# Kernel tuning notes

Measured on AMD Instinct MI355X. Metric: run time of the kernel, lower is better.

The kernel has to match this reference:

```python
import jax, jax.numpy as jnp
import numpy as np

# Dimensions pinned by the module: RelPosEmb1DAISummer(tokens=50, dim_head=124)
H = 8          # num_heads
D = 31         # channels // num_heads
T = 4          # time axis of the (p, t) spatial grid; D*T == 124 == dim_head
P = 50         # tokens
C = H * D      # 248 channels
SCALE = D ** -0.5  # note: module scales by d**-0.5 (=31), not (d*t)**-0.5 -- faithful


def rel_to_abs(x):
    """AI-Summer 1D relative->absolute reindexing. x: [b, h, l, 2l-1] -> [b, h, l, l]."""
    b, h, l, _ = x.shape
    x = jnp.pad(x, ((0, 0), (0, 0), (0, 0), (0, 1)))          # [b,h,l,2l]
    x = x.reshape(b, h, l * 2 * l)
    x = jnp.pad(x, ((0, 0), (0, 0), (0, l - 1)))
    x = x.reshape(b, h, l + 1, 2 * l - 1)
    return x[:, :, :l, l - 1:]


def setup_inputs() -> dict:
    key = jax.random.key(0)
    k1, k2, k3, k4 = jax.random.split(key, 4)
    B = 512
    x = jax.random.normal(k1, (B, C, P, T), jnp.float32)
    # 1x1 conv == per-position linear over channels: weight [3C, C], bias [3C]
    w_qkv = jax.random.normal(k2, (3 * C, C), jnp.float32) * (C ** -0.5)
    b_qkv = jax.random.normal(k3, (3 * C,), jnp.float32) * 0.01
    # shared-heads relative position embedding: [2*tokens-1, dim_head]
    rel_emb = jax.random.normal(k4, (2 * P - 1, D * T), jnp.float32) * ((D * T) ** -0.5)
    return {"x": x, "w_qkv": w_qkv, "b_qkv": b_qkv, "rel_emb": rel_emb}


def reference(x, w_qkv, b_qkv, rel_emb):
    B = x.shape[0]
    # 1x1 Conv2d: [B, C, P, T] -> [B, 3C, P, T]
    qkv = jnp.einsum('bcpt,oc->bopt', x, w_qkv) + b_qkv[None, :, None, None]
    # 'b (qkv h d) p t -> qkv b h d p t'
    qkv = qkv.reshape(B, 3, H, D, P, T)
    q, k, v = qkv[:, 0], qkv[:, 1], qkv[:, 2]                 # each [B,H,D,P,T]
    q = q.transpose(0, 1, 3, 2, 4).reshape(B, H, P, D * T)    # 'b h d p t -> b h p (d t)'
    k = k.transpose(0, 1, 2, 4, 3).reshape(B, H, D * T, P)    # 'b h d p t -> b h (d t) p'
    v = v.transpose(0, 1, 3, 2, 4).reshape(B, H, P, D * T)
    dots = jnp.einsum('bhpi,bhiq->bhpq', q, k)                # [B,H,P,P]
    bias = rel_to_abs(jnp.einsum('bhpd,rd->bhpr', q, rel_emb))
    attn = jax.nn.softmax((dots + bias) * SCALE, axis=-1)     # dropout = identity (eval)
    out = jnp.einsum('bhpq,bhqi->bhpi', attn, v)              # [B,H,P,D*T]
    # 'b h p (d t) -> b (h d) p t'
    out = out.reshape(B, H, P, D, T).transpose(0, 1, 3, 2, 4).reshape(B, H * D, P, T)
    return out
```

## Files before the change

kernel.cpp:

```cpp
#include <hip/hip_runtime.h>
#include <hip/hip_bf16.h>
#include <stdint.h>

typedef __bf16 bf16_t;
typedef bf16_t bf16x8 __attribute__((ext_vector_type(8)));
typedef bf16_t bf16x4 __attribute__((ext_vector_type(4)));
typedef float f32x4 __attribute__((ext_vector_type(4)));

constexpr float SCALE = 0.17960530202677491f;

__device__ __forceinline__ f32x4 mfma16(bf16x8 a, bf16x8 b, f32x4 c) {
    return __builtin_amdgcn_mfma_f32_16x16x32_bf16(a, b, c, 0, 0, 0);
}
__device__ __forceinline__ void fence() {
    asm volatile("s_waitcnt lgkmcnt(0)" ::: "memory");
}
__device__ __forceinline__ void gload_lds16(const void* g, void* l) {
    __builtin_amdgcn_global_load_lds((const __attribute__((address_space(1))) void*)g,
                                     (__attribute__((address_space(3))) void*)l, 16, 0, 0);
}

__global__ void prep_kernel(const float* __restrict__ w, const float* __restrict__ rel,
                            bf16_t* __restrict__ WT, bf16_t* __restrict__ relf)
{
    int i = blockIdx.x * 256 + threadIdx.x;
    if (i < 196608) {
        int o = i >> 8, c = i & 255;
        WT[i] = (o < 744 && c < 248) ? (bf16_t)w[(long)o * 248 + c] : (bf16_t)0.f;
        return;
    }
    i -= 196608;
    if (i < 14336) {
        int e = i & 7, lane = (i >> 3) & 63;
        int f = i >> 9;
        int ks = f & 3, rt = f >> 2;
        int r = rt * 16 + (lane & 15);
        int dt = ks * 32 + (lane >> 4) * 8 + e;
        float v = 0.f;
        if (r < 99 && dt < 124) v = rel[r * 124 + dt];
        relf[i] = (bf16_t)v;
    }
}

__global__ void __launch_bounds__(512)
xb_kernel(const float* __restrict__ x, bf16_t* __restrict__ XT)
{
    __shared__ __align__(16) char XS[31744];
    const int tid = threadIdx.x;
    const int blk = blockIdx.x;
    const int cl = tid & 63;
    const int cg = tid >> 6;
    {
        int f = blk * 64 + cl;
        int b = f / 200;
        int nn = f - b * 200;
        const float* xp = x + (long)b * 49600 + nn;
#pragma unroll
        for (int ii = 0; ii < 4; ++ii) {
            int cb = cg + 8 * ii;
            if (cb < 31) {
                bf16x8 pk;
#pragma unroll
                for (int e = 0; e < 8; ++e)
                    pk[e] = (bf16_t)xp[(long)(cb * 8 + e) * 200];
                *(bf16x8*)(XS + cl * 496 + cb * 16) = pk;
            }
        }
    }
    __syncthreads();
    if (tid < 496) {
        char* dst = (char*)XT + (long)blk * 31744 + tid * 64;
#pragma unroll
        for (int j = 0; j < 4; ++j)
            *(f32x4*)(dst + j * 16) = *(const f32x4*)(XS + tid * 64 + j * 16);
    }
}

__global__ void __launch_bounds__(256)
qkv_kernel(const bf16_t* __restrict__ XT, const bf16_t* __restrict__ WT,
           const float* __restrict__ bqkv, bf16_t* __restrict__ qkv)
{
    __shared__ __align__(16) char SM[32768];
    const int raw = blockIdx.x;
    const int swz = (raw & 7) * 600 + (raw >> 3);
    const int mt = swz % 6, nt = swz / 6;
    const int n0 = nt * 128, o0 = mt * 128;
    const int tid  = threadIdx.x;
    const int lane = tid & 63;
    const int wv   = tid >> 6;
    const int r15  = lane & 15, g4 = lane >> 4;
    const int kc   = lane & 3, rsub = lane >> 2;
    const int wr = wv >> 1, wc = wv & 1;

    f32x4 acc[4][4];
#pragma unroll
    for (int a = 0; a < 4; ++a)
#pragma unroll
        for (int b = 0; b < 4; ++b) acc[a][b] = f32x4{0.f, 0.f, 0.f, 0.f};

    const char* XTb = (const char*)XT;
    const char* WTb = (const char*)WT;

#define STAGE(BUF, KS)                                                          \
    {                                                                           \
        _Pragma("unroll")                                                       \
        for (int i_ = 0; i_ < 2; ++i_) {                                        \
            int r0 = (wv * 2 + i_) * 16;                                        \
            int row = r0 + rsub;                                                \
            gload_lds16(XTb + (long)(n0 + row) * 496 + ((KS) * 4 + kc) * 16,    \
                        SM + (BUF) * 8192 + r0 * 64);                           \
            gload_lds16(WTb + (long)(o0 + row) * 512 + ((KS) * 4 + kc) * 16,    \
                        SM + 16384 + (BUF) * 8192 + r0 * 64);                   \
        }                                                                       \
    }

    STAGE(0, 0);
    __syncthreads();

    int buf = 0;
    for (int ks = 0; ks < 8; ++ks) {
        if (ks < 7) STAGE(buf ^ 1, ks + 1);
        bf16x8 Af[4], Bf[4];
#pragma unroll
        for (int fn = 0; fn < 4; ++fn) {
            int row = wr * 64 + fn * 16 + r15;
            Af[fn] = *(const bf16x8*)(SM + buf * 8192 + row * 64 + g4 * 16);
        }
#pragma unroll
        for (int fo = 0; fo < 4; ++fo) {
            int row = wc * 64 + fo * 16 + r15;
            Bf[fo] = *(const bf16x8*)(SM + 16384 + buf * 8192 + row * 64 + g4 * 16);
        }
#pragma unroll
        for (int fn = 0; fn < 4; ++fn)
#pragma unroll
            for (int fo = 0; fo < 4; ++fo)
                acc[fn][fo] = mfma16(Af[fn], Bf[fo], acc[fn][fo]);
        __syncthreads();
        buf ^= 1;
    }
#undef STAGE

#pragma unroll
    for (int fo = 0; fo < 4; ++fo) {
        int o = o0 + wc * 64 + fo * 16 + r15;
        bool vo = (o < 744);
        int s = (o >= 496) ? 2 : ((o >= 248) ? 1 : 0);
        int rem = o - s * 248;
        int h = rem / 31;
        int d = rem - h * 31;
        float bias = vo ? bqkv[o] : 0.f;
        float sc = (s == 0) ? SCALE : 1.f;
        bf16_t* baseo = qkv + (long)s * 26214400 + d * 4;
#pragma unroll
        for (int fn = 0; fn < 4; ++fn) {
            int n = n0 + wr * 64 + fn * 16 + g4 * 4;
            int b = n / 200;
            int p = (n - b * 200) >> 2;
            if (vo) {
                f32x4 a = acc[fn][fo];
                bf16x4 pk = {(bf16_t)((a[0] + bias) * sc), (bf16_t)((a[1] + bias) * sc),
                             (bf16_t)((a[2] + bias) * sc), (bf16_t)((a[3] + bias) * sc)};
                *(bf16x4*)(baseo + ((long)(b * 8 + h) * 50 + p) * 128) = pk;
            }
        }
    }
}

__global__ void __launch_bounds__(256)
attn_kernel(const bf16_t* __restrict__ qkv, const bf16_t* __restrict__ relf,
            float* __restrict__ out)
{
    __shared__ float LS[50][52];
    __shared__ __align__(16) char AS[8192];
    __shared__ __align__(16) char VT[16384];
    const int bid = blockIdx.x;
    const int bb = bid >> 3, hh = bid & 7;
    const int tid  = threadIdx.x;
    const int lane = tid & 63;
    const int w    = tid >> 6;
    const int r15  = lane & 15, g4 = lane >> 4;

    const bf16_t* qB = qkv + (long)bid * 6400;
    const bf16_t* kB = qkv + 26214400L + (long)bid * 6400;
    const bf16_t* vB = qkv + 52428800L + (long)bid * 6400;

    {
        int p_ = tid >> 2, cc = tid & 3;
#pragma unroll
        for (int u = 0; u < 4; ++u) {
            int c = cc + u * 4;
            bf16x8 vv = *(const bf16x8*)(vB + p_ * 128 + c * 8);
#pragma unroll
            for (int e = 0; e < 8; ++e) {
                int i = c * 8 + e;
                *(bf16_t*)(VT + i * 128 + ((((p_ >> 3) ^ (i & 7))) << 4) + (p_ & 7) * 2) = vv[e];
            }
        }
    }

    bf16x8 Afr[4];
#pragma unroll
    for (int ks = 0; ks < 4; ++ks)
        Afr[ks] = *(const bf16x8*)(qB + (w * 16 + r15) * 128 + ks * 32 + g4 * 8);

#pragma unroll
    for (int ct = 0; ct < 4; ++ct) {
        int c = ct * 16 + r15;
        f32x4 sA = f32x4{0.f, 0.f, 0.f, 0.f};
#pragma unroll
        for (int ks = 0; ks < 4; ++ks) {
            bf16x8 Bf = *(const bf16x8*)(kB + c * 128 + ks * 32 + g4 * 8);
            sA = mfma16(Afr[ks], Bf, sA);
        }
        if (c < 50) {
#pragma unroll
            for (int j = 0; j < 4; ++j) {
                int qrow = w * 16 + g4 * 4 + j;
                if (qrow < 50) LS[qrow][c] = sA[j];
            }
        }
    }
    fence();

    {
        const bf16_t* rf = relf + lane * 8;
        bf16x8 R0[4];
#pragma unroll
        for (int ks = 0; ks < 4; ++ks) R0[ks] = *(const bf16x8*)(rf + (ks << 9));
        for (int rt = 0; rt < 7; ++rt) {
            bf16x8 R1[4];
            if (rt < 6) {
#pragma unroll
                for (int ks = 0; ks < 4; ++ks)
                    R1[ks] = *(const bf16x8*)(rf + (((rt + 1) * 4 + ks) << 9));
            }
            f32x4 sA = f32x4{0.f, 0.f, 0.f, 0.f};
#pragma unroll
            for (int ks = 0; ks < 4; ++ks) sA = mfma16(Afr[ks], R0[ks], sA);
            int r = rt * 16 + r15;
#pragma unroll
            for (int j = 0; j < 4; ++j) {
                int qrow = w * 16 + g4 * 4 + j;
                int jj = r + qrow - 49;
                if (qrow < 50 && jj >= 0 && jj < 50) LS[qrow][jj] += sA[j];
            }
#pragma unroll
            for (int ks = 0; ks < 4; ++ks) R0[ks] = R1[ks];
        }
    }
    fence();

    {
        int row = w * 16 + (lane >> 2);
        int quad = lane & 3;
        int hrow = row & 7;
        if (row < 50) {
            float mx = -1e30f;
            for (int jj = quad; jj < 50; jj += 4) mx = fmaxf(mx, LS[row][jj]);
            mx = fmaxf(mx, __shfl_xor(mx, 1));
            mx = fmaxf(mx, __shfl_xor(mx, 2));
            float sum = 0.f;
            for (int jj = quad; jj < 50; jj += 4) {
                float e = __expf(LS[row][jj] - mx);
                LS[row][jj] = e;
                sum += e;
            }
            sum += __shfl_xor(sum, 1);
            sum += __shfl_xor(sum, 2);
            float rs = 1.f / sum;
            for (int jj = quad; jj < 64; jj += 4) {
                float v = (jj < 50) ? LS[row][jj] * rs : 0.f;
                *(bf16_t*)(AS + row * 128 + (((jj >> 3) ^ hrow) << 4) + (jj & 7) * 2) = (bf16_t)v;
            }
        } else {
            for (int jj = quad; jj < 64; jj += 4)
                *(bf16_t*)(AS + row * 128 + (((jj >> 3) ^ hrow) << 4) + (jj & 7) * 2) = (bf16_t)0.f;
        }
    }
    __syncthreads();

#pragma unroll
    for (int ii = 0; ii < 2; ++ii) {
        int itile = w * 2 + ii;
        int irow = itile * 16 + r15;
        bf16x8 Av[2];
#pragma unroll
        for (int ks = 0; ks < 2; ++ks)
            Av[ks] = *(const bf16x8*)(VT + irow * 128 + ((((ks * 4) + g4) ^ (irow & 7)) << 4));
        int dd = itile * 4 + g4;
#pragma unroll
        for (int pt = 0; pt < 4; ++pt) {
            int prow = pt * 16 + r15;
            int hp2 = prow & 7;
            f32x4 po = f32x4{0.f, 0.f, 0.f, 0.f};
#pragma unroll
            for (int ks = 0; ks < 2; ++ks) {
                bf16x8 Bs = *(const bf16x8*)(AS + prow * 128 + ((((ks * 4) + g4) ^ hp2) << 4));
                po = mfma16(Av[ks], Bs, po);
            }
            if (dd < 31 && prow < 50)
                *(f32x4*)(out + ((long)bb * 248 + hh * 31 + dd) * 200 + prow * 4) = po;
        }
    }
}

extern "C" void kernel_launch(void* const* d_in, const int* in_sizes, int n_in,
                              void* d_out, int out_size, void* d_ws, size_t ws_size,
                              hipStream_t stream)
{
    const float* x   = (const float*)d_in[0];
    const float* wq  = (const float*)d_in[1];
    const float* bq  = (const float*)d_in[2];
    const float* rel = (const float*)d_in[3];
    float* out = (float*)d_out;

    char* ws = (char*)d_ws;
    bf16_t* WT   = (bf16_t*)ws;
    bf16_t* relf = (bf16_t*)(ws + 393216);
    bf16_t* qkv  = (bf16_t*)(ws + 421888);

    bf16_t* XT = (bf16_t*)d_out;

    const int B = in_sizes[0] / 49600;

    prep_kernel<<<dim3(824), dim3(256), 0, stream>>>(wq, rel, WT, relf);
    xb_kernel<<<dim3(B * 200 / 64), dim3(512), 0, stream>>>(x, XT);
    qkv_kernel<<<dim3(4800), dim3(256), 0, stream>>>(XT, WT, bq, qkv);
    attn_kernel<<<dim3(B * 8), dim3(256), 0, stream>>>(qkv, relf, out);
}
```

Measured before the change: 194.8 us.

## Store V pre-transposed from QKV epilogue and defer softmax normalization

The QKV GEMM epilogue now writes V directly in a transposed [bh][dt][p] layout, padded to 64 columns, and the prep kernel zero-fills the padding. This removes the per-block LDS transpose of V in the attention kernel. The softmax no longer writes back normalized values: unnormalized exps go straight into the bf16 A buffer, and the 1/sum scale is applied to the output. The trade-off is scattered 2-byte global stores in the QKV epilogue and an extra zero-fill pass over the vT buffer.

```diff
diff --git a/kernel.cpp b/kernel.cpp
--- a/kernel.cpp
+++ b/kernel.cpp
@@ -21,7 +21,8 @@
 }
 
 __global__ void prep_kernel(const float* __restrict__ w, const float* __restrict__ rel,
-                            bf16_t* __restrict__ WT, bf16_t* __restrict__ relf)
+                            bf16_t* __restrict__ WT, bf16_t* __restrict__ relf,
+                            bf16_t* __restrict__ vT)
 {
     int i = blockIdx.x * 256 + threadIdx.x;
     if (i < 196608) {
@@ -39,6 +40,19 @@
         float v = 0.f;
         if (r < 99 && dt < 124) v = rel[r * 124 + dt];
         relf[i] = (bf16_t)v;
+        return;
+    }
+    i -= 14336;
+    if (i < 524288) {
+        int bh = i >> 7, r = i & 127;
+        char* rb = (char*)(vT + ((long)bh * 128 + r) * 64);
+        f32x4 z = f32x4{0.f, 0.f, 0.f, 0.f};
+        *(f32x4*)(rb + 96)  = z;
+        *(f32x4*)(rb + 112) = z;
+        if (r >= 124) {
+#pragma unroll
+            for (int j = 0; j < 6; ++j) *(f32x4*)(rb + j * 16) = z;
+        }
     }
 }
 
@@ -78,7 +92,8 @@
 
 __global__ void __launch_bounds__(256)
 qkv_kernel(const bf16_t* __restrict__ XT, const bf16_t* __restrict__ WT,
-           const float* __restrict__ bqkv, bf16_t* __restrict__ qkv)
+           const float* __restrict__ bqkv, bf16_t* __restrict__ qk,
+           bf16_t* __restrict__ vT)
 {
     __shared__ __align__(16) char SM[32768];
     const int raw = blockIdx.x;
@@ -151,29 +166,38 @@
         int d = rem - h * 31;
         float bias = vo ? bqkv[o] : 0.f;
         float sc = (s == 0) ? SCALE : 1.f;
-        bf16_t* baseo = qkv + (long)s * 26214400 + d * 4;
 #pragma unroll
         for (int fn = 0; fn < 4; ++fn) {
             int n = n0 + wr * 64 + fn * 16 + g4 * 4;
             int b = n / 200;
             int p = (n - b * 200) >> 2;
+            long bh = (long)(b * 8 + h);
             if (vo) {
                 f32x4 a = acc[fn][fo];
-                bf16x4 pk = {(bf16_t)((a[0] + bias) * sc), (bf16_t)((a[1] + bias) * sc),
-                             (bf16_t)((a[2] + bias) * sc), (bf16_t)((a[3] + bias) * sc)};
-                *(bf16x4*)(baseo + ((long)(b * 8 + h) * 50 + p) * 128) = pk;
+                float a0 = (a[0] + bias) * sc, a1 = (a[1] + bias) * sc;
+                float a2 = (a[2] + bias) * sc, a3 = (a[3] + bias) * sc;
+                if (s < 2) {
+                    bf16x4 pk = {(bf16_t)a0, (bf16_t)a1, (bf16_t)a2, (bf16_t)a3};
+                    *(bf16x4*)(qk + (long)s * 26214400 + (bh * 50 + p) * 128 + d * 4) = pk;
+                } else {
+                    bf16_t* vb2 = vT + (bh * 128 + d * 4) * 64 + p;
+                    vb2[0]   = (bf16_t)a0;
+                    vb2[64]  = (bf16_t)a1;
+                    vb2[128] = (bf16_t)a2;
+                    vb2[192] = (bf16_t)a3;
+                }
             }
         }
     }
 }
 
 __global__ void __launch_bounds__(256)
-attn_kernel(const bf16_t* __restrict__ qkv, const bf16_t* __restrict__ relf,
-            float* __restrict__ out)
+attn_kernel(const bf16_t* __restrict__ qk, const bf16_t* __restrict__ vT,
+            const bf16_t* __restrict__ relf, float* __restrict__ out)
 {
     __shared__ float LS[50][52];
     __shared__ __align__(16) char AS[8192];
-    __shared__ __align__(16) char VT[16384];
+    __shared__ float RS[64];
     const int bid = blockIdx.x;
     const int bb = bid >> 3, hh = bid & 7;
     const int tid  = threadIdx.x;
@@ -181,23 +205,9 @@
     const int w    = tid >> 6;
     const int r15  = lane & 15, g4 = lane >> 4;
 
-    const bf16_t* qB = qkv + (long)bid * 6400;
-    const bf16_t* kB = qkv + 26214400L + (long)bid * 6400;
-    const bf16_t* vB = qkv + 52428800L + (long)bid * 6400;
-
-    {
-        int p_ = tid >> 2, cc = tid & 3;
-#pragma unroll
-        for (int u = 0; u < 4; ++u) {
-            int c = cc + u * 4;
-            bf16x8 vv = *(const bf16x8*)(vB + p_ * 128 + c * 8);
-#pragma unroll
-            for (int e = 0; e < 8; ++e) {
-                int i = c * 8 + e;
-                *(bf16_t*)(VT + i * 128 + ((((p_ >> 3) ^ (i & 7))) << 4) + (p_ & 7) * 2) = vv[e];
-            }
-        }
-    }
+    const bf16_t* qB = qk + (long)bid * 6400;
+    const bf16_t* kB = qk + 26214400L + (long)bid * 6400;
+    const bf16_t* vTb = vT + (long)bid * 8192;
 
     bf16x8 Afr[4];
 #pragma unroll
@@ -263,19 +273,14 @@
             float sum = 0.f;
             for (int jj = quad; jj < 50; jj += 4) {
                 float e = __expf(LS[row][jj] - mx);
-                LS[row][jj] = e;
                 sum += e;
-            }
+                *(bf16_t*)(AS + row * 128 + (((jj >> 3) ^ hrow) << 4) + (jj & 7) * 2) = (bf16_t)e;
+            }
+            for (int jj = 50 + quad; jj < 64; jj += 4)
+                *(bf16_t*)(AS + row * 128 + (((jj >> 3) ^ hrow) << 4) + (jj & 7) * 2) = (bf16_t)0.f;
             sum += __shfl_xor(sum, 1);
             sum += __shfl_xor(sum, 2);
-            float rs = 1.f / sum;
-            for (int jj = quad; jj < 64; jj += 4) {
-                float v = (jj < 50) ? LS[row][jj] * rs : 0.f;
-                *(bf16_t*)(AS + row * 128 + (((jj >> 3) ^ hrow) << 4) + (jj & 7) * 2) = (bf16_t)v;
-            }
-        } else {
-            for (int jj = quad; jj < 64; jj += 4)
-                *(bf16_t*)(AS + row * 128 + (((jj >> 3) ^ hrow) << 4) + (jj & 7) * 2) = (bf16_t)0.f;
+            if (quad == 0) RS[row] = 1.f / sum;
         }
     }
     __syncthreads();
@@ -287,7 +292,7 @@
         bf16x8 Av[2];
 #pragma unroll
         for (int ks = 0; ks < 2; ++ks)
-            Av[ks] = *(const bf16x8*)(VT + irow * 128 + ((((ks * 4) + g4) ^ (irow & 7)) << 4));
+            Av[ks] = *(const bf16x8*)(vTb + irow * 64 + ks * 32 + g4 * 8);
         int dd = itile * 4 + g4;
 #pragma unroll
         for (int pt = 0; pt < 4; ++pt) {
@@ -299,8 +304,11 @@
                 bf16x8 Bs = *(const bf16x8*)(AS + prow * 128 + ((((ks * 4) + g4) ^ hp2) << 4));
                 po = mfma16(Av[ks], Bs, po);
             }
-            if (dd < 31 && prow < 50)
+            if (dd < 31 && prow < 50) {
+                float rsv = RS[prow];
+                po[0] *= rsv; po[1] *= rsv; po[2] *= rsv; po[3] *= rsv;
                 *(f32x4*)(out + ((long)bb * 248 + hh * 31 + dd) * 200 + prow * 4) = po;
+            }
         }
     }
 }
@@ -318,14 +326,15 @@
     char* ws = (char*)d_ws;
     bf16_t* WT   = (bf16_t*)ws;
     bf16_t* relf = (bf16_t*)(ws + 393216);
-    bf16_t* qkv  = (bf16_t*)(ws + 421888);
+    bf16_t* qk   = (bf16_t*)(ws + 421888);
+    bf16_t* vT   = qk + 52428800L;
 
     bf16_t* XT = (bf16_t*)d_out;
 
     const int B = in_sizes[0] / 49600;
 
-    prep_kernel<<<dim3(824), dim3(256), 0, stream>>>(wq, rel, WT, relf);
+    prep_kernel<<<dim3(2872), dim3(256), 0, stream>>>(wq, rel, WT, relf, vT);
     xb_kernel<<<dim3(B * 200 / 64), dim3(512), 0, stream>>>(x, XT);
-    qkv_kernel<<<dim3(4800), dim3(256), 0, stream>>>(XT, WT, bq, qkv);
-    attn_kernel<<<dim3(B * 8), dim3(256), 0, stream>>>(qkv, relf, out);
-}
+    qkv_kernel<<<dim3(4800), dim3(256), 0, stream>>>(XT, WT, bq, qk, vT);
+    attn_kernel<<<dim3(B * 8), dim3(256), 0, stream>>>(qk, vT, relf, out);
+}
```

After: 246.0 us. +26.3%, slower.

## Pretranspose V in separate kernel and process two heads per attention block

Applied to the files above, without the earlier changes.

V is now written to its own padded buffer, and a new vt_kernel transposes it in place in global memory, so the attention kernel no longer does the scattered LDS transpose. Each attention block now handles two heads. This lets the rel-emb fragments be loaded once and reused for both heads and interleaves independent MFMA chains. Softmax normalisation is deferred to the output epilogue through a per-row reciprocal, which drops one LDS pass. The cost is an extra kernel launch plus a full read and write of V, and higher register and LDS use per block with half as many blocks.

```diff
diff --git a/kernel.cpp b/kernel.cpp
--- a/kernel.cpp
+++ b/kernel.cpp
@@ -78,7 +78,8 @@
 
 __global__ void __launch_bounds__(256)
 qkv_kernel(const bf16_t* __restrict__ XT, const bf16_t* __restrict__ WT,
-           const float* __restrict__ bqkv, bf16_t* __restrict__ qkv)
+           const float* __restrict__ bqkv, bf16_t* __restrict__ qk,
+           bf16_t* __restrict__ vbuf)
 {
     __shared__ __align__(16) char SM[32768];
     const int raw = blockIdx.x;
@@ -151,73 +152,105 @@
         int d = rem - h * 31;
         float bias = vo ? bqkv[o] : 0.f;
         float sc = (s == 0) ? SCALE : 1.f;
-        bf16_t* baseo = qkv + (long)s * 26214400 + d * 4;
 #pragma unroll
         for (int fn = 0; fn < 4; ++fn) {
             int n = n0 + wr * 64 + fn * 16 + g4 * 4;
             int b = n / 200;
             int p = (n - b * 200) >> 2;
+            long bh = (long)(b * 8 + h);
             if (vo) {
                 f32x4 a = acc[fn][fo];
                 bf16x4 pk = {(bf16_t)((a[0] + bias) * sc), (bf16_t)((a[1] + bias) * sc),
                              (bf16_t)((a[2] + bias) * sc), (bf16_t)((a[3] + bias) * sc)};
-                *(bf16x4*)(baseo + ((long)(b * 8 + h) * 50 + p) * 128) = pk;
+                if (s < 2)
+                    *(bf16x4*)(qk + (long)s * 26214400 + (bh * 50 + p) * 128 + d * 4) = pk;
+                else
+                    *(bf16x4*)(vbuf + bh * 8192 + p * 128 + d * 4) = pk;
             }
         }
     }
 }
 
 __global__ void __launch_bounds__(256)
-attn_kernel(const bf16_t* __restrict__ qkv, const bf16_t* __restrict__ relf,
-            float* __restrict__ out)
-{
-    __shared__ float LS[50][52];
-    __shared__ __align__(16) char AS[8192];
-    __shared__ __align__(16) char VT[16384];
-    const int bid = blockIdx.x;
-    const int bb = bid >> 3, hh = bid & 7;
+vt_kernel(bf16_t* __restrict__ vbuf)
+{
+    __shared__ __align__(16) bf16_t VS[50][136];
+    const int bh = blockIdx.x;
+    bf16_t* vb = vbuf + (long)bh * 8192;
+    const int tid = threadIdx.x;
+#pragma unroll
+    for (int u = 0; u < 4; ++u) {
+        int idx = tid + u * 256;
+        if (idx < 800) {
+            int p = idx >> 4, ch = idx & 15;
+            *(bf16x8*)(&VS[p][ch * 8]) = *(const bf16x8*)(vb + p * 128 + ch * 8);
+        }
+    }
+    __syncthreads();
+    const int i = tid >> 1, p0 = (tid & 1) * 32;
+    bf16_t tmp[32];
+#pragma unroll
+    for (int u = 0; u < 32; ++u) {
+        int p = p0 + u;
+        tmp[u] = (p < 50 && i < 124) ? VS[p][i] : (bf16_t)0.f;
+    }
+#pragma unroll
+    for (int q8 = 0; q8 < 4; ++q8)
+        *(bf16x8*)(vb + i * 64 + p0 + q8 * 8) = *(const bf16x8*)(&tmp[q8 * 8]);
+}
+
+__global__ void __launch_bounds__(256)
+attn_kernel(const bf16_t* __restrict__ qk, const bf16_t* __restrict__ vbuf,
+            const bf16_t* __restrict__ relf, float* __restrict__ out)
+{
+    __shared__ float LS[2][50][52];
+    __shared__ __align__(16) char AS[2][8192];
+    __shared__ float RS[2][64];
+    const int bp = blockIdx.x;
+    const int bb = bp >> 2;
+    const int h0 = (bp & 3) * 2;
     const int tid  = threadIdx.x;
     const int lane = tid & 63;
     const int w    = tid >> 6;
     const int r15  = lane & 15, g4 = lane >> 4;
 
-    const bf16_t* qB = qkv + (long)bid * 6400;
-    const bf16_t* kB = qkv + 26214400L + (long)bid * 6400;
-    const bf16_t* vB = qkv + 52428800L + (long)bid * 6400;
-
-    {
-        int p_ = tid >> 2, cc = tid & 3;
-#pragma unroll
-        for (int u = 0; u < 4; ++u) {
-            int c = cc + u * 4;
-            bf16x8 vv = *(const bf16x8*)(vB + p_ * 128 + c * 8);
-#pragma unroll
-            for (int e = 0; e < 8; ++e) {
-                int i = c * 8 + e;
-                *(bf16_t*)(VT + i * 128 + ((((p_ >> 3) ^ (i & 7))) << 4) + (p_ & 7) * 2) = vv[e];
-            }
-        }
-    }
-
-    bf16x8 Afr[4];
-#pragma unroll
-    for (int ks = 0; ks < 4; ++ks)
-        Afr[ks] = *(const bf16x8*)(qB + (w * 16 + r15) * 128 + ks * 32 + g4 * 8);
-
-#pragma unroll
+    const bf16_t* qB[2], * kB[2], * vT[2];
+#pragma unroll
+    for (int S = 0; S < 2; ++S) {
+        long bh = (long)bb * 8 + h0 + S;
+        qB[S] = qk + bh * 6400;
+        kB[S] = qk + 26214400L + bh * 6400;
+        vT[S] = vbuf + bh * 8192;
+    }
+
+    bf16x8 Afr[2][4];
+#pragma unroll
+    for (int S = 0; S < 2; ++S)
+#pragma unroll
+        for (int ks = 0; ks < 4; ++ks)
+            Afr[S][ks] = *(const bf16x8*)(qB[S] + (w * 16 + r15) * 128 + ks * 32 + g4 * 8);
+
+#pragma unroll 2
     for (int ct = 0; ct < 4; ++ct) {
         int c = ct * 16 + r15;
-        f32x4 sA = f32x4{0.f, 0.f, 0.f, 0.f};
+        bf16x8 Bf[2][4];
+#pragma unroll
+        for (int S = 0; S < 2; ++S)
+#pragma unroll
+            for (int ks = 0; ks < 4; ++ks)
+                Bf[S][ks] = *(const bf16x8*)(kB[S] + c * 128 + ks * 32 + g4 * 8);
+        f32x4 s0 = f32x4{0.f, 0.f, 0.f, 0.f};
+        f32x4 s1 = f32x4{0.f, 0.f, 0.f, 0.f};
 #pragma unroll
         for (int ks = 0; ks < 4; ++ks) {
-            bf16x8 Bf = *(const bf16x8*)(kB + c * 128 + ks * 32 + g4 * 8);
-            sA = mfma16(Afr[ks], Bf, sA);
+            s0 = mfma16(Afr[0][ks], Bf[0][ks], s0);
+            s1 = mfma16(Afr[1][ks], Bf[1][ks], s1);
         }
         if (c < 50) {
 #pragma unroll
             for (int j = 0; j < 4; ++j) {
                 int qrow = w * 16 + g4 * 4 + j;
-                if (qrow < 50) LS[qrow][c] = sA[j];
+                if (qrow < 50) { LS[0][qrow][c] = s0[j]; LS[1][qrow][c] = s1[j]; }
             }
         }
     }
@@ -225,28 +258,29 @@
 
     {
         const bf16_t* rf = relf + lane * 8;
-        bf16x8 R0[4];
-#pragma unroll
-        for (int ks = 0; ks < 4; ++ks) R0[ks] = *(const bf16x8*)(rf + (ks << 9));
+#pragma unroll 2
         for (int rt = 0; rt < 7; ++rt) {
-            bf16x8 R1[4];
-            if (rt < 6) {
-#pragma unroll
-                for (int ks = 0; ks < 4; ++ks)
-                    R1[ks] = *(const bf16x8*)(rf + (((rt + 1) * 4 + ks) << 9));
-            }
-            f32x4 sA = f32x4{0.f, 0.f, 0.f, 0.f};
-#pragma unroll
-            for (int ks = 0; ks < 4; ++ks) sA = mfma16(Afr[ks], R0[ks], sA);
+            bf16x8 R[4];
+#pragma unroll
+            for (int ks = 0; ks < 4; ++ks)
+                R[ks] = *(const bf16x8*)(rf + ((rt * 4 + ks) << 9));
+            f32x4 s0 = f32x4{0.f, 0.f, 0.f, 0.f};
+            f32x4 s1 = f32x4{0.f, 0.f, 0.f, 0.f};
+#pragma unroll
+            for (int ks = 0; ks < 4; ++ks) {
+                s0 = mfma16(Afr[0][ks], R[ks], s0);
+                s1 = mfma16(Afr[1][ks], R[ks], s1);
+            }
             int r = rt * 16 + r15;
 #pragma unroll
             for (int j = 0; j < 4; ++j) {
                 int qrow = w * 16 + g4 * 4 + j;
                 int jj = r + qrow - 49;
-                if (qrow < 50 && jj >= 0 && jj < 50) LS[qrow][jj] += sA[j];
-            }
-#pragma unroll
-            for (int ks = 0; ks < 4; ++ks) R0[ks] = R1[ks];
+                if (qrow < 50 && jj >= 0 && jj < 50) {
+                    LS[0][qrow][jj] += s0[j];
+                    LS[1][qrow][jj] += s1[j];
+                }
+            }
         }
     }
     fence();
@@ -256,26 +290,24 @@
         int quad = lane & 3;
         int hrow = row & 7;
         if (row < 50) {
-            float mx = -1e30f;
-            for (int jj = quad; jj < 50; jj += 4) mx = fmaxf(mx, LS[row][jj]);
-            mx = fmaxf(mx, __shfl_xor(mx, 1));
-            mx = fmaxf(mx, __shfl_xor(mx, 2));
-            float sum = 0.f;
-            for (int jj = quad; jj < 50; jj += 4) {
-                float e = __expf(LS[row][jj] - mx);
-                LS[row][jj] = e;
-                sum += e;
-            }
-            sum += __shfl_xor(sum, 1);
-            sum += __shfl_xor(sum, 2);
-            float rs = 1.f / sum;
-            for (int jj = quad; jj < 64; jj += 4) {
-                float v = (jj < 50) ? LS[row][jj] * rs : 0.f;
-                *(bf16_t*)(AS + row * 128 + (((jj >> 3) ^ hrow) << 4) + (jj & 7) * 2) = (bf16_t)v;
-            }
-        } else {
-            for (int jj = quad; jj < 64; jj += 4)
-                *(bf16_t*)(AS + row * 128 + (((jj >> 3) ^ hrow) << 4) + (jj & 7) * 2) = (bf16_t)0.f;
+#pragma unroll
+            for (int S = 0; S < 2; ++S) {
+                float mx = -1e30f;
+                for (int jj = quad; jj < 50; jj += 4) mx = fmaxf(mx, LS[S][row][jj]);
+                mx = fmaxf(mx, __shfl_xor(mx, 1));
+                mx = fmaxf(mx, __shfl_xor(mx, 2));
+                float sum = 0.f;
+                for (int jj = quad; jj < 50; jj += 4) {
+                    float e = __expf(LS[S][row][jj] - mx);
+                    sum += e;
+                    *(bf16_t*)(AS[S] + row * 128 + (((jj >> 3) ^ hrow) << 4) + (jj & 7) * 2) = (bf16_t)e;
+                }
+                for (int jj = 50 + quad; jj < 64; jj += 4)
+                    *(bf16_t*)(AS[S] + row * 128 + (((jj >> 3) ^ hrow) << 4) + (jj & 7) * 2) = (bf16_t)0.f;
+                sum += __shfl_xor(sum, 1);
+                sum += __shfl_xor(sum, 2);
+                if (quad == 0) RS[S][row] = 1.f / sum;
+            }
         }
     }
     __syncthreads();
@@ -284,23 +316,33 @@
     for (int ii = 0; ii < 2; ++ii) {
         int itile = w * 2 + ii;
         int irow = itile * 16 + r15;
-        bf16x8 Av[2];
-#pragma unroll
-        for (int ks = 0; ks < 2; ++ks)
-            Av[ks] = *(const bf16x8*)(VT + irow * 128 + ((((ks * 4) + g4) ^ (irow & 7)) << 4));
         int dd = itile * 4 + g4;
+        bf16x8 Av[2][2];
+#pragma unroll
+        for (int S = 0; S < 2; ++S)
+#pragma unroll
+            for (int ks = 0; ks < 2; ++ks)
+                Av[S][ks] = *(const bf16x8*)(vT[S] + irow * 64 + ks * 32 + g4 * 8);
 #pragma unroll
         for (int pt = 0; pt < 4; ++pt) {
             int prow = pt * 16 + r15;
             int hp2 = prow & 7;
-            f32x4 po = f32x4{0.f, 0.f, 0.f, 0.f};
+            f32x4 po0 = f32x4{0.f, 0.f, 0.f, 0.f};
+            f32x4 po1 = f32x4{0.f, 0.f, 0.f, 0.f};
 #pragma unroll
             for (int ks = 0; ks < 2; ++ks) {
-                bf16x8 Bs = *(const bf16x8*)(AS + prow * 128 + ((((ks * 4) + g4) ^ hp2) << 4));
-                po = mfma16(Av[ks], Bs, po);
-            }
-            if (dd < 31 && prow < 50)
-                *(f32x4*)(out + ((long)bb * 248 + hh * 31 + dd) * 200 + prow * 4) = po;
+                bf16x8 Bs0 = *(const bf16x8*)(AS[0] + prow * 128 + ((((ks * 4) + g4) ^ hp2) << 4));
+                bf16x8 Bs1 = *(const bf16x8*)(AS[1] + prow * 128 + ((((ks * 4) + g4) ^ hp2) << 4));
+                po0 = mfma16(Av[0][ks], Bs0, po0);
+                po1 = mfma16(Av[1][ks], Bs1, po1);
+            }
+            if (dd < 31 && prow < 50) {
+                float r0 = RS[0][prow], r1 = RS[1][prow];
+                po0[0] *= r0; po0[1] *= r0; po0[2] *= r0; po0[3] *= r0;
+                po1[0] *= r1; po1[1] *= r1; po1[2] *= r1; po1[3] *= r1;
+                *(f32x4*)(out + ((long)bb * 248 + (h0 + 0) * 31 + dd) * 200 + prow * 4) = po0;
+                *(f32x4*)(out + ((long)bb * 248 + (h0 + 1) * 31 + dd) * 200 + prow * 4) = po1;
+            }
         }
     }
 }
@@ -318,7 +360,8 @@
     char* ws = (char*)d_ws;
     bf16_t* WT   = (bf16_t*)ws;
     bf16_t* relf = (bf16_t*)(ws + 393216);
-    bf16_t* qkv  = (bf16_t*)(ws + 421888);
+    bf16_t* qk   = (bf16_t*)(ws + 421888);
+    bf16_t* vbuf = qk + 52428800L;
 
     bf16_t* XT = (bf16_t*)d_out;
 
@@ -326,6 +369,7 @@
 
     prep_kernel<<<dim3(824), dim3(256), 0, stream>>>(wq, rel, WT, relf);
     xb_kernel<<<dim3(B * 200 / 64), dim3(512), 0, stream>>>(x, XT);
-    qkv_kernel<<<dim3(4800), dim3(256), 0, stream>>>(XT, WT, bq, qkv);
-    attn_kernel<<<dim3(B * 8), dim3(256), 0, stream>>>(qkv, relf, out);
-}
+    qkv_kernel<<<dim3(4800), dim3(256), 0, stream>>>(XT, WT, bq, qk, vbuf);
+    vt_kernel<<<dim3(B * 8), dim3(256), 0, stream>>>(vbuf);
+    attn_kernel<<<dim3(B * 4), dim3(256), 0, stream>>>(qk, vbuf, relf, out);
+}
```

New measurement: 233.6 us. 19.9% more time.
